# Performance work log

Measured on AMD Instinct MI355X. Metric: run time of the kernel, lower is better.

## Reference

```python
import jax, jax.numpy as jnp
import numpy as np
import math
from jax import lax

K = 5
PAD = K // 2
TAU = 0.1
ALPHA = 2.0
BETA = 1.0
MAXH = math.log(K * K - 1)


def _logp(f):
    # f: [B, d, H, W]; normalize along channels, local kxk affinities (center excluded), log_softmax
    B, d, H, W = f.shape
    nrm = jnp.sqrt(jnp.sum(f * f, axis=1, keepdims=True))
    fn = f / jnp.maximum(nrm, 1e-12)
    fp = jnp.pad(fn, ((0, 0), (0, 0), (PAD, PAD), (PAD, PAD)), mode='reflect')
    center = K * K // 2
    affs = []
    for i in range(K):
        for j in range(K):
            if i * K + j == center:
                continue  # mask removes the center neighbor
            affs.append(jnp.einsum('bdhw,bdhw->bhw', fn, fp[:, :, i:i + H, j:j + W]))
    aff = jnp.stack(affs, axis=-1).reshape(B, H * W, K * K - 1)
    return jax.nn.log_softmax(aff / TAU, axis=-1)


def _sobel_mag(x):
    # x: [B, C, H, W] -> [B, H*W] edge magnitude, per-image min-max normalized
    xm = jnp.mean(x, axis=1, keepdims=True)
    kx = jnp.array([[-1., 0., 1.], [-2., 0., 2.], [-1., 0., 1.]], dtype=x.dtype).reshape(1, 1, 3, 3)
    ky = jnp.array([[-1., -2., -1.], [0., 0., 0.], [1., 2., 1.]], dtype=x.dtype).reshape(1, 1, 3, 3)
    dn = ('NCHW', 'OIHW', 'NCHW')
    gx = lax.conv_general_dilated(xm, kx, (1, 1), 'SAME', dimension_numbers=dn)
    gy = lax.conv_general_dilated(xm, ky, (1, 1), 'SAME', dimension_numbers=dn)
    m = jnp.sqrt(gx * gx + gy * gy)[:, 0]
    mn = jnp.min(m, axis=(1, 2), keepdims=True)
    mx = jnp.max(m, axis=(1, 2), keepdims=True)
    m = (m - mn) / (mx - mn + 1e-6)
    return m.reshape(m.shape[0], -1)


def setup_inputs() -> dict:
    key = jax.random.key(0)
    k1, k2, k3, k4 = jax.random.split(key, 4)
    fs3 = jax.random.normal(k1, (8, 256, 64, 64), dtype=jnp.float32)
    ft = jax.random.normal(k2, (8, 512, 32, 32), dtype=jnp.float32)
    Ws = jax.random.normal(k3, (64, 256), dtype=jnp.float32) / np.sqrt(256.0)
    Wt = jax.random.normal(k4, (64, 512), dtype=jnp.float32) / np.sqrt(512.0)
    return {"fs3": fs3, "ft": ft, "Ws": Ws, "Wt": Wt}


def reference(fs3, ft, Ws, Wt):
    B, _, H, W = fs3.shape
    # bilinear, align_corners=False (half-pixel) == jax.image.resize 'bilinear'
    ft_r = jax.image.resize(ft, (ft.shape[0], ft.shape[1], H, W), method='bilinear')
    s = jnp.einsum('oc,bchw->bohw', Ws, fs3)   # 1x1 conv, no bias
    t = jnp.einsum('oc,bchw->bohw', Wt, ft_r)
    t_logp = _logp(t)
    s_logp = _logp(s)
    # gating weights computed under no_grad in the original
    t_logp_ng = lax.stop_gradient(t_logp)
    t_p = jnp.exp(t_logp_ng)
    ent = -jnp.sum(t_p * t_logp_ng, axis=-1)
    w_conf = jnp.clip(1.0 - ent / (MAXH + 1e-12), 0.0, 1.0)
    w_edge = _sobel_mag(lax.stop_gradient(t))
    w = w_conf ** ALPHA * (1.0 + BETA * w_edge)
    # zero out pad-wide border
    m = jnp.pad(jnp.ones((B, H - 2 * PAD, W - 2 * PAD), dtype=fs3.dtype),
                ((0, 0), (PAD, PAD), (PAD, PAD)))
    w = lax.stop_gradient(w * m.reshape(B, -1))
    kl = jnp.sum(t_p * (t_logp - s_logp), axis=-1)
    return jnp.sum(w * kl) / (jnp.sum(w) + 1e-6)
```

## Files before the change

kernel.cpp:

```cpp
#include <hip/hip_runtime.h>
#include <math.h>


#define WS_T32   0u
#define WS_TN    2097152u
#define WS_SN    4194304u
#define WS_TM    6291456u
#define WS_MAG   6324224u
#define WS_WTT   6356992u
#define WS_WST   6389760u
#define WS_MNMX  6406144u
#define WS_ACC   6406160u
#define WS_SLOGP 0u

static __device__ __forceinline__ int reflect_idx(int i, int n) {
  if (i < 0) i = -i;
  if (i >= n) i = 2 * n - 2 - i;
  return i;
}

__global__ __launch_bounds__(256) void k_transw(const float* __restrict__ Wt,
                                                const float* __restrict__ Ws,
                                                float* __restrict__ WtT,
                                                float* __restrict__ WsT,
                                                unsigned int* __restrict__ mnmx,
                                                double* __restrict__ accg) {
  if (blockIdx.x == 0) {
    int t = threadIdx.x;
    if (t < 8) mnmx[t] = 0x7F800000u;
    else if (t < 16) mnmx[t] = 0u;
    else if (t == 16) { accg[0] = 0.0; accg[1] = 0.0; }
  }
  int idx = blockIdx.x * 256 + threadIdx.x;
  if (idx < 32768) {
    int o = idx >> 9, c = idx & 511;
    WtT[c * 64 + o] = Wt[idx];
  } else {
    int j = idx - 32768;
    int o = j >> 8, c = j & 255;
    WsT[c * 64 + o] = Ws[j];
  }
}

__global__ __launch_bounds__(256) void k_gemm_t(const float* __restrict__ ft,
                                                const float* __restrict__ WtT,
                                                float* __restrict__ t32p) {
  const int tid = threadIdx.x;
  const int wvu = __builtin_amdgcn_readfirstlane(tid >> 6);
  const int ln = tid & 63;
  const int p = blockIdx.x * 64 + ln;
  const int b = p >> 10, pix = p & 1023;
  const int cbase = blockIdx.y * 128;
  float ac[16];
#pragma unroll
  for (int i = 0; i < 16; i++) ac[i] = 0.f;
  const float* ftb = ft + ((size_t)b * 512 + cbase) * 1024 + pix;
  const float* wp = WtT + (size_t)cbase * 64 + wvu * 16;
  for (int c = 0; c < 128; c += 4) {
    float v0 = ftb[(size_t)(c + 0) * 1024];
    float v1 = ftb[(size_t)(c + 1) * 1024];
    float v2 = ftb[(size_t)(c + 2) * 1024];
    float v3 = ftb[(size_t)(c + 3) * 1024];
#pragma unroll
    for (int o = 0; o < 16; o++)
      ac[o] += wp[(c + 0) * 64 + o] * v0 + wp[(c + 1) * 64 + o] * v1
             + wp[(c + 2) * 64 + o] * v2 + wp[(c + 3) * 64 + o] * v3;
  }
  float4* outp = (float4*)(t32p + (size_t)blockIdx.y * 524288
                           + ((size_t)b * 1024 + pix) * 64 + wvu * 16);
#pragma unroll
  for (int j = 0; j < 4; j++)
    outp[j] = make_float4(ac[4 * j], ac[4 * j + 1], ac[4 * j + 2], ac[4 * j + 3]);
}

__global__ __launch_bounds__(128) void k_resize_norm(const float* __restrict__ t32p,
                                                     float* __restrict__ tn,
                                                     float* __restrict__ tm) {
  const int p = blockIdx.x * 128 + threadIdx.x;
  const int b = p >> 12, pix = p & 4095;
  const int y = pix >> 6, x = pix & 63;
  float fy = 0.5f * y - 0.25f, fx = 0.5f * x - 0.25f;
  int y0f = (int)floorf(fy), x0f = (int)floorf(fx);
  float wy = fy - (float)y0f, wx = fx - (float)x0f;
  int y1 = min(y0f + 1, 31), x1 = min(x0f + 1, 31);
  int y0 = max(y0f, 0), x0 = max(x0f, 0);
  const int ip[4] = {y0 * 32 + x0, y0 * 32 + x1, y1 * 32 + x0, y1 * 32 + x1};
  const float wg[4] = {(1.f - wy) * (1.f - wx), (1.f - wy) * wx, wy * (1.f - wx), wy * wx};
  float v[64];
#pragma unroll
  for (int i = 0; i < 64; i++) v[i] = 0.f;
#pragma unroll
  for (int q = 0; q < 4; q++) {
    const float* src = t32p + ((size_t)b * 1024 + ip[q]) * 64;
    float wq = wg[q];
#pragma unroll
    for (int part = 0; part < 4; part++) {
      const float4* s4 = (const float4*)(src + (size_t)part * 524288);
#pragma unroll
      for (int cg = 0; cg < 16; cg++) {
        float4 f = s4[cg];
        v[4 * cg + 0] += wq * f.x; v[4 * cg + 1] += wq * f.y;
        v[4 * cg + 2] += wq * f.z; v[4 * cg + 3] += wq * f.w;
      }
    }
  }
  float sum = 0.f, ssq = 0.f;
#pragma unroll
  for (int i = 0; i < 64; i++) { sum += v[i]; ssq += v[i] * v[i]; }
  float rn = 1.f / fmaxf(sqrtf(ssq), 1e-12f);
  float4* tnp = (float4*)(tn + ((size_t)b * 4096 + pix) * 64);
#pragma unroll
  for (int cg = 0; cg < 16; cg++)
    tnp[cg] = make_float4(v[4 * cg] * rn, v[4 * cg + 1] * rn, v[4 * cg + 2] * rn, v[4 * cg + 3] * rn);
  tm[p] = sum * (1.f / 64.f);
}

__global__ __launch_bounds__(128) void k_sobel(const float* __restrict__ tm,
                                               float* __restrict__ mag,
                                               unsigned int* __restrict__ mnmx) {
  const int p = blockIdx.x * 128 + threadIdx.x;
  const int b = p >> 12, pix = p & 4095;
  const int y = pix >> 6, x = pix & 63;
  const float* img = tm + (size_t)b * 4096;
  float v[3][3];
#pragma unroll
  for (int r = -1; r <= 1; r++)
#pragma unroll
    for (int c = -1; c <= 1; c++) {
      int yy = y + r, xx = x + c;
      v[r + 1][c + 1] = (yy >= 0 && yy < 64 && xx >= 0 && xx < 64) ? img[yy * 64 + xx] : 0.f;
    }
  float gx = (v[0][2] - v[0][0]) + 2.f * (v[1][2] - v[1][0]) + (v[2][2] - v[2][0]);
  float gy = (v[2][0] - v[0][0]) + 2.f * (v[2][1] - v[0][1]) + (v[2][2] - v[0][2]);
  float m = sqrtf(gx * gx + gy * gy);
  mag[p] = m;
  unsigned int mu = __float_as_uint(m);
  unsigned int mnu = mu, mxu = mu;
#pragma unroll
  for (int off = 32; off >= 1; off >>= 1) {
    mnu = min(mnu, __shfl_xor(mnu, off));
    mxu = max(mxu, __shfl_xor(mxu, off));
  }
  if ((threadIdx.x & 63) == 0) {
    atomicMin(&mnmx[b], mnu);
    atomicMax(&mnmx[8 + b], mxu);
  }
}

__global__ __launch_bounds__(256) void k_gemm_s(const float* __restrict__ fs3,
                                                const float* __restrict__ WsT,
                                                float* __restrict__ sn) {
  __shared__ float ssq_l[4][64];
  const int tid = threadIdx.x;
  const int wvu = __builtin_amdgcn_readfirstlane(tid >> 6);
  const int ln = tid & 63;
  const int p = blockIdx.x * 64 + ln;
  const int b = p >> 12, pix = p & 4095;
  float ac[16];
#pragma unroll
  for (int i = 0; i < 16; i++) ac[i] = 0.f;
  const float* fb = fs3 + (size_t)b * 256 * 4096 + pix;
  const float* wp = WsT + wvu * 16;
  for (int c = 0; c < 256; c += 4) {
    float v0 = fb[(size_t)(c + 0) * 4096];
    float v1 = fb[(size_t)(c + 1) * 4096];
    float v2 = fb[(size_t)(c + 2) * 4096];
    float v3 = fb[(size_t)(c + 3) * 4096];
#pragma unroll
    for (int o = 0; o < 16; o++)
      ac[o] += wp[(c + 0) * 64 + o] * v0 + wp[(c + 1) * 64 + o] * v1
             + wp[(c + 2) * 64 + o] * v2 + wp[(c + 3) * 64 + o] * v3;
  }
  float ss = 0.f;
#pragma unroll
  for (int i = 0; i < 16; i++) ss += ac[i] * ac[i];
  ssq_l[wvu][ln] = ss;
  __syncthreads();
  float tot = ssq_l[0][ln] + ssq_l[1][ln] + ssq_l[2][ln] + ssq_l[3][ln];
  float rn = 1.f / fmaxf(sqrtf(tot), 1e-12f);
  float4* ob = (float4*)(sn + ((size_t)b * 4096 + pix) * 64 + wvu * 16);
#pragma unroll
  for (int j = 0; j < 4; j++)
    ob[j] = make_float4(ac[4 * j] * rn, ac[4 * j + 1] * rn, ac[4 * j + 2] * rn, ac[4 * j + 3] * rn);
}

template <int TPASS>
__global__ __launch_bounds__(256) void k_aff(const float* __restrict__ fn,
                                             float* __restrict__ slogp,
                                             const float* __restrict__ mag,
                                             const unsigned int* __restrict__ mnmx,
                                             double* __restrict__ accg) {
  __shared__ __align__(16) float fl[144 * 68];
  const int tid = threadIdx.x;
  const int wvu = __builtin_amdgcn_readfirstlane(tid >> 6);
  const int ln = tid & 63;
  const int b = blockIdx.x >> 6, tl = blockIdx.x & 63;
  const int ty0 = (tl >> 3) * 8, tx0 = (tl & 7) * 8;
  const int ty = ln >> 3, tx = ln & 7;
#pragma unroll
  for (int i = 0; i < 9; i++) {
    int flat = i * 256 + tid;
    int pos = flat >> 4, cg = flat & 15;
    int hy = pos / 12, hx = pos - hy * 12;
    int gy2 = reflect_idx(ty0 + hy - 2, 64);
    int gx2 = reflect_idx(tx0 + hx - 2, 64);
    float4 f = *(const float4*)(fn + ((size_t)b * 4096 + gy2 * 64 + gx2) * 64 + cg * 4);
    int sw = (((pos * 17) >> 3) & 3) << 2;
    *(float4*)(&fl[pos * 68 + ((cg * 4) ^ sw)]) = f;
  }
  __syncthreads();
  const int base = ty * 12 + tx;
  const int cbase = wvu * 16;
  float4 cv[4];
  {
    int cp = base + 26;
    int cs = (((cp * 17) >> 3) & 3) << 2;
    const float* crow = &fl[cp * 68];
#pragma unroll
    for (int j = 0; j < 4; j++) cv[j] = *(const float4*)(crow + ((cbase + 4 * j) ^ cs));
  }
  float aff[24];
  {
    int n = 0;
#pragma unroll
    for (int dy = 0; dy < 5; dy++)
#pragma unroll
      for (int dx = 0; dx < 5; dx++) {
        if (dy == 2 && dx == 2) continue;
        int pp = base + dy * 12 + dx;
        int sw2 = (((pp * 17) >> 3) & 3) << 2;
        const float* rowp = &fl[pp * 68];
        float4 n0 = *(const float4*)(rowp + ((cbase + 0) ^ sw2));
        float4 n1 = *(const float4*)(rowp + ((cbase + 4) ^ sw2));
        float4 n2 = *(const float4*)(rowp + ((cbase + 8) ^ sw2));
        float4 n3 = *(const float4*)(rowp + ((cbase + 12) ^ sw2));
        aff[n] = cv[0].x * n0.x + cv[0].y * n0.y + cv[0].z * n0.z + cv[0].w * n0.w
               + cv[1].x * n1.x + cv[1].y * n1.y + cv[1].z * n1.z + cv[1].w * n1.w
               + cv[2].x * n2.x + cv[2].y * n2.y + cv[2].z * n2.z + cv[2].w * n2.w
               + cv[3].x * n3.x + cv[3].y * n3.y + cv[3].z * n3.z + cv[3].w * n3.w;
        n++;
      }
  }
  __syncthreads();
  float* r = fl;
#pragma unroll
  for (int n = 0; n < 24; n++) r[(wvu * 64 + ln) * 25 + n] = aff[n];
  __syncthreads();
  if (wvu != 0) return;
  float a[24];
#pragma unroll
  for (int n = 0; n < 24; n++)
    a[n] = r[ln * 25 + n] + r[(64 + ln) * 25 + n] + r[(128 + ln) * 25 + n] + r[(192 + ln) * 25 + n];
  float mxa = a[0];
#pragma unroll
  for (int n = 1; n < 24; n++) mxa = fmaxf(mxa, a[n]);
  float e[24]; float sum = 0.f;
#pragma unroll
  for (int n = 0; n < 24; n++) { e[n] = expf((a[n] - mxa) * 10.f); sum += e[n]; }
  float lse = logf(sum);
  const int gy = ty0 + ty, gx = tx0 + tx;
  const int gpix = b * 4096 + gy * 64 + gx;
  if (TPASS == 0) {
#pragma unroll
    for (int n = 0; n < 24; n++)
      slogp[(size_t)n * 32768 + gpix] = (a[n] - mxa) * 10.f - lse;
  } else {
    float rs = 1.f / sum;
    float ent = 0.f, kl = 0.f;
#pragma unroll
    for (int n = 0; n < 24; n++) {
      float tp = e[n] * rs;
      float tlp = (a[n] - mxa) * 10.f - lse;
      ent -= tp * tlp;
      kl += tp * (tlp - slogp[(size_t)n * 32768 + gpix]);
    }
    float wconf = 1.f - ent * (1.0f / 3.17805383034794580f);
    wconf = fminf(fmaxf(wconf, 0.f), 1.f);
    float mnv = __uint_as_float(mnmx[b]);
    float mxv = __uint_as_float(mnmx[8 + b]);
    float wedge = (mag[gpix] - mnv) / (mxv - mnv + 1e-6f);
    float w = wconf * wconf * (1.f + wedge);
    if (gy < 2 || gy >= 62 || gx < 2 || gx >= 62) w = 0.f;
    double wkl = (double)(w * kl), wsum = (double)w;
#pragma unroll
    for (int off = 32; off >= 1; off >>= 1) {
      wkl  += __shfl_down(wkl, off);
      wsum += __shfl_down(wsum, off);
    }
    if (ln == 0) { atomicAdd(&accg[0], wkl); atomicAdd(&accg[1], wsum); }
  }
}

__global__ void k_final(const double* __restrict__ accg, float* __restrict__ out) {
  out[0] = (float)(accg[0] / (accg[1] + 1e-6));
}

extern "C" void kernel_launch(void* const* d_in, const int* in_sizes, int n_in,
                              void* d_out, int out_size, void* d_ws, size_t ws_size,
                              hipStream_t stream) {
  const float* fs3 = (const float*)d_in[0];
  const float* ft  = (const float*)d_in[1];
  const float* Ws  = (const float*)d_in[2];
  const float* Wt  = (const float*)d_in[3];
  float* out = (float*)d_out;
  float* w = (float*)d_ws;
  float* t32   = w + WS_T32;
  float* tn    = w + WS_TN;
  float* sn    = w + WS_SN;
  float* tm    = w + WS_TM;
  float* mag   = w + WS_MAG;
  float* WtT   = w + WS_WTT;
  float* WsT   = w + WS_WST;
  float* slogp = w + WS_SLOGP;
  unsigned int* mnmx = (unsigned int*)(w + WS_MNMX);
  double* acc = (double*)(w + WS_ACC);

  k_transw<<<192, 256, 0, stream>>>(Wt, Ws, WtT, WsT, mnmx, acc);
  k_gemm_t<<<dim3(128, 4), 256, 0, stream>>>(ft, WtT, t32);
  k_resize_norm<<<256, 128, 0, stream>>>(t32, tn, tm);
  k_sobel<<<256, 128, 0, stream>>>(tm, mag, mnmx);
  k_gemm_s<<<512, 256, 0, stream>>>(fs3, WsT, sn);
  k_aff<0><<<512, 256, 0, stream>>>(sn, slogp, nullptr, nullptr, nullptr);
  k_aff<1><<<512, 256, 0, stream>>>(tn, slogp, mag, mnmx, acc);
  k_final<<<1, 1, 0, stream>>>(acc, out);
}
```

Measured before the change: 201.4 us.

## Fuse student/teacher affinity passes, restructure GEMMs and resize, drop final kernel

Merges the two affinity passes into one kernel that stages both student and teacher halos in shared memory. This removes the slogp round trip through global memory and one launch. The final division moves into the last block via an atomic counter, so the separate k_final launch goes away. Both 1x1-conv GEMMs now use 512-thread blocks with 8 outputs per wave and register double-buffered weight and input loads, and the teacher GEMM writes channel-major output. The resize kernel uses 4 threads per pixel with shuffle reductions. The risks are more shared memory per block, which lowers occupancy, and extra atomic ordering logic.

```diff
diff --git a/kernel.cpp b/kernel.cpp
--- a/kernel.cpp
+++ b/kernel.cpp
@@ -10,8 +10,7 @@
 #define WS_WTT   6356992u
 #define WS_WST   6389760u
 #define WS_MNMX  6406144u
-#define WS_ACC   6406160u
-#define WS_SLOGP 0u
+#define WS_ACC   6406168u
 
 static __device__ __forceinline__ int reflect_idx(int i, int n) {
   if (i < 0) i = -i;
@@ -29,7 +28,9 @@
     int t = threadIdx.x;
     if (t < 8) mnmx[t] = 0x7F800000u;
     else if (t < 16) mnmx[t] = 0u;
-    else if (t == 16) { accg[0] = 0.0; accg[1] = 0.0; }
+    else if (t == 16) mnmx[16] = 0u;
+    else if (t == 17) accg[0] = 0.0;
+    else if (t == 18) accg[1] = 0.0;
   }
   int idx = blockIdx.x * 256 + threadIdx.x;
   if (idx < 32768) {
@@ -42,41 +43,66 @@
   }
 }
 
-__global__ __launch_bounds__(256) void k_gemm_t(const float* __restrict__ ft,
-                                                const float* __restrict__ WtT,
-                                                float* __restrict__ t32p) {
+#define LW(WB, CC, A0, A1, B0, B1, C0, C1, D0, D1)                         \
+  { const float4* q0 = (const float4*)((WB) + (CC) * 64);       A0 = q0[0]; A1 = q0[1]; \
+    const float4* q1 = (const float4*)((WB) + ((CC) + 1) * 64); B0 = q1[0]; B1 = q1[1]; \
+    const float4* q2 = (const float4*)((WB) + ((CC) + 2) * 64); C0 = q2[0]; C1 = q2[1]; \
+    const float4* q3 = (const float4*)((WB) + ((CC) + 3) * 64); D0 = q3[0]; D1 = q3[1]; }
+
+#define FMA_GROUP(AC)                                                       \
+  { AC[0] += w00.x * v0 + w10.x * v1 + w20.x * v2 + w30.x * v3;             \
+    AC[1] += w00.y * v0 + w10.y * v1 + w20.y * v2 + w30.y * v3;             \
+    AC[2] += w00.z * v0 + w10.z * v1 + w20.z * v2 + w30.z * v3;             \
+    AC[3] += w00.w * v0 + w10.w * v1 + w20.w * v2 + w30.w * v3;             \
+    AC[4] += w01.x * v0 + w11.x * v1 + w21.x * v2 + w31.x * v3;             \
+    AC[5] += w01.y * v0 + w11.y * v1 + w21.y * v2 + w31.y * v3;             \
+    AC[6] += w01.z * v0 + w11.z * v1 + w21.z * v2 + w31.z * v3;             \
+    AC[7] += w01.w * v0 + w11.w * v1 + w21.w * v2 + w31.w * v3; }
+
+#define ROT8() { w00 = x00; w01 = x01; w10 = x10; w11 = x11;                \
+                 w20 = x20; w21 = x21; w30 = x30; w31 = x31;                \
+                 v0 = u0; v1 = u1; v2 = u2; v3 = u3; }
+
+__global__ __launch_bounds__(512, 4) void k_gemm_t(const float* __restrict__ ft,
+                                                   const float* __restrict__ WtT,
+                                                   float* __restrict__ t32p) {
   const int tid = threadIdx.x;
-  const int wvu = __builtin_amdgcn_readfirstlane(tid >> 6);
-  const int ln = tid & 63;
-  const int p = blockIdx.x * 64 + ln;
-  const int b = p >> 10, pix = p & 1023;
-  const int cbase = blockIdx.y * 128;
-  float ac[16];
-#pragma unroll
-  for (int i = 0; i < 16; i++) ac[i] = 0.f;
-  const float* ftb = ft + ((size_t)b * 512 + cbase) * 1024 + pix;
-  const float* wp = WtT + (size_t)cbase * 64 + wvu * 16;
+  const int w = tid >> 6, ln = tid & 63;
+  const int o0 = __builtin_amdgcn_readfirstlane(w * 8);
+  const int bx = blockIdx.x;
+  const int b = bx >> 4;
+  const int pixl = (bx & 15) * 64 + ln;
+  const int part = blockIdx.y;
+  const float* fb = ft + (size_t)b * 524288 + (size_t)(part * 128) * 1024 + pixl;
+  const float* wb = WtT + (part * 128) * 64 + o0;
+  float ac[8];
+#pragma unroll
+  for (int j = 0; j < 8; j++) ac[j] = 0.f;
+  float4 w00, w01, w10, w11, w20, w21, w30, w31;
+  float v0, v1, v2, v3;
+  LW(wb, 0, w00, w01, w10, w11, w20, w21, w30, w31);
+  { const float* f = fb; v0 = f[0]; v1 = f[1024]; v2 = f[2048]; v3 = f[3072]; }
   for (int c = 0; c < 128; c += 4) {
-    float v0 = ftb[(size_t)(c + 0) * 1024];
-    float v1 = ftb[(size_t)(c + 1) * 1024];
-    float v2 = ftb[(size_t)(c + 2) * 1024];
-    float v3 = ftb[(size_t)(c + 3) * 1024];
-#pragma unroll
-    for (int o = 0; o < 16; o++)
-      ac[o] += wp[(c + 0) * 64 + o] * v0 + wp[(c + 1) * 64 + o] * v1
-             + wp[(c + 2) * 64 + o] * v2 + wp[(c + 3) * 64 + o] * v3;
-  }
-  float4* outp = (float4*)(t32p + (size_t)blockIdx.y * 524288
-                           + ((size_t)b * 1024 + pix) * 64 + wvu * 16);
-#pragma unroll
-  for (int j = 0; j < 4; j++)
-    outp[j] = make_float4(ac[4 * j], ac[4 * j + 1], ac[4 * j + 2], ac[4 * j + 3]);
-}
-
-__global__ __launch_bounds__(128) void k_resize_norm(const float* __restrict__ t32p,
-                                                     float* __restrict__ tn,
-                                                     float* __restrict__ tm) {
-  const int p = blockIdx.x * 128 + threadIdx.x;
+    float4 x00 = {0,0,0,0}, x01 = x00, x10 = x00, x11 = x00, x20 = x00, x21 = x00, x30 = x00, x31 = x00;
+    float u0 = 0.f, u1 = 0.f, u2 = 0.f, u3 = 0.f;
+    if (c + 4 < 128) {
+      LW(wb, c + 4, x00, x01, x10, x11, x20, x21, x30, x31);
+      const float* f = fb + (size_t)(c + 4) * 1024;
+      u0 = f[0]; u1 = f[1024]; u2 = f[2048]; u3 = f[3072];
+    }
+    FMA_GROUP(ac);
+    ROT8();
+  }
+  float* ob = t32p + (((size_t)part * 8 + b) * 64 + o0) * 1024 + pixl;
+#pragma unroll
+  for (int j = 0; j < 8; j++) ob[(size_t)j * 1024] = ac[j];
+}
+
+__global__ __launch_bounds__(256, 4) void k_resize_norm(const float* __restrict__ t32p,
+                                                        float* __restrict__ tn,
+                                                        float* __restrict__ tm) {
+  const int g = blockIdx.x * 256 + threadIdx.x;
+  const int p = g >> 2, q = g & 3;
   const int b = p >> 12, pix = p & 4095;
   const int y = pix >> 6, x = pix & 63;
   float fy = 0.5f * y - 0.25f, fx = 0.5f * x - 0.25f;
@@ -86,33 +112,31 @@
   int y0 = max(y0f, 0), x0 = max(x0f, 0);
   const int ip[4] = {y0 * 32 + x0, y0 * 32 + x1, y1 * 32 + x0, y1 * 32 + x1};
   const float wg[4] = {(1.f - wy) * (1.f - wx), (1.f - wy) * wx, wy * (1.f - wx), wy * wx};
-  float v[64];
-#pragma unroll
-  for (int i = 0; i < 64; i++) v[i] = 0.f;
-#pragma unroll
-  for (int q = 0; q < 4; q++) {
-    const float* src = t32p + ((size_t)b * 1024 + ip[q]) * 64;
-    float wq = wg[q];
+  float v[16];
+#pragma unroll
+  for (int i = 0; i < 16; i++) v[i] = 0.f;
+#pragma unroll
+  for (int cr = 0; cr < 4; cr++) {
+    float wq = wg[cr];
 #pragma unroll
     for (int part = 0; part < 4; part++) {
-      const float4* s4 = (const float4*)(src + (size_t)part * 524288);
-#pragma unroll
-      for (int cg = 0; cg < 16; cg++) {
-        float4 f = s4[cg];
-        v[4 * cg + 0] += wq * f.x; v[4 * cg + 1] += wq * f.y;
-        v[4 * cg + 2] += wq * f.z; v[4 * cg + 3] += wq * f.w;
-      }
+      const float* base = t32p + (((size_t)part * 8 + b) * 64 + q * 16) * 1024 + ip[cr];
+#pragma unroll
+      for (int c = 0; c < 16; c++) v[c] += wq * base[(size_t)c * 1024];
     }
   }
   float sum = 0.f, ssq = 0.f;
 #pragma unroll
-  for (int i = 0; i < 64; i++) { sum += v[i]; ssq += v[i] * v[i]; }
-  float rn = 1.f / fmaxf(sqrtf(ssq), 1e-12f);
-  float4* tnp = (float4*)(tn + ((size_t)b * 4096 + pix) * 64);
-#pragma unroll
-  for (int cg = 0; cg < 16; cg++)
-    tnp[cg] = make_float4(v[4 * cg] * rn, v[4 * cg + 1] * rn, v[4 * cg + 2] * rn, v[4 * cg + 3] * rn);
-  tm[p] = sum * (1.f / 64.f);
+  for (int i = 0; i < 16; i++) { sum += v[i]; ssq += v[i] * v[i]; }
+  float s1 = sum + __shfl_xor(sum, 1);  float sumf = s1 + __shfl_xor(s1, 2);
+  float q1 = ssq + __shfl_xor(ssq, 1);  float ssqf = q1 + __shfl_xor(q1, 2);
+  float rn = 1.f / fmaxf(sqrtf(ssqf), 1e-12f);
+  float* tp = tn + ((size_t)b * 4096 + pix) * 64 + q * 16;
+#pragma unroll
+  for (int j = 0; j < 4; j++)
+    *(float4*)(tp + 4 * j) = make_float4(v[4 * j] * rn, v[4 * j + 1] * rn,
+                                         v[4 * j + 2] * rn, v[4 * j + 3] * rn);
+  if (q == 0) tm[p] = sumf * (1.f / 64.f);
 }
 
 __global__ __launch_bounds__(128) void k_sobel(const float* __restrict__ tm,
@@ -147,50 +171,89 @@
   }
 }
 
-__global__ __launch_bounds__(256) void k_gemm_s(const float* __restrict__ fs3,
-                                                const float* __restrict__ WsT,
-                                                float* __restrict__ sn) {
-  __shared__ float ssq_l[4][64];
+__global__ __launch_bounds__(512, 4) void k_gemm_s(const float* __restrict__ fs3,
+                                                   const float* __restrict__ WsT,
+                                                   float* __restrict__ sn) {
+  __shared__ float ssq_l[8][64];
   const int tid = threadIdx.x;
-  const int wvu = __builtin_amdgcn_readfirstlane(tid >> 6);
-  const int ln = tid & 63;
-  const int p = blockIdx.x * 64 + ln;
-  const int b = p >> 12, pix = p & 4095;
-  float ac[16];
-#pragma unroll
-  for (int i = 0; i < 16; i++) ac[i] = 0.f;
-  const float* fb = fs3 + (size_t)b * 256 * 4096 + pix;
-  const float* wp = WsT + wvu * 16;
+  const int w = tid >> 6, ln = tid & 63;
+  const int o0 = __builtin_amdgcn_readfirstlane(w * 8);
+  const int bx = blockIdx.x;
+  const int b = bx >> 6;
+  const int pixl = (bx & 63) * 64 + ln;
+  const float* fb = fs3 + (size_t)b * 1048576 + pixl;
+  const float* wb = WsT + o0;
+  float ac[8];
+#pragma unroll
+  for (int j = 0; j < 8; j++) ac[j] = 0.f;
+  float4 w00, w01, w10, w11, w20, w21, w30, w31;
+  float v0, v1, v2, v3;
+  LW(wb, 0, w00, w01, w10, w11, w20, w21, w30, w31);
+  { const float* f = fb; v0 = f[0]; v1 = f[4096]; v2 = f[8192]; v3 = f[12288]; }
   for (int c = 0; c < 256; c += 4) {
-    float v0 = fb[(size_t)(c + 0) * 4096];
-    float v1 = fb[(size_t)(c + 1) * 4096];
-    float v2 = fb[(size_t)(c + 2) * 4096];
-    float v3 = fb[(size_t)(c + 3) * 4096];
-#pragma unroll
-    for (int o = 0; o < 16; o++)
-      ac[o] += wp[(c + 0) * 64 + o] * v0 + wp[(c + 1) * 64 + o] * v1
-             + wp[(c + 2) * 64 + o] * v2 + wp[(c + 3) * 64 + o] * v3;
+    float4 x00 = {0,0,0,0}, x01 = x00, x10 = x00, x11 = x00, x20 = x00, x21 = x00, x30 = x00, x31 = x00;
+    float u0 = 0.f, u1 = 0.f, u2 = 0.f, u3 = 0.f;
+    if (c + 4 < 256) {
+      LW(wb, c + 4, x00, x01, x10, x11, x20, x21, x30, x31);
+      const float* f = fb + (size_t)(c + 4) * 4096;
+      u0 = f[0]; u1 = f[4096]; u2 = f[8192]; u3 = f[12288];
+    }
+    FMA_GROUP(ac);
+    ROT8();
   }
   float ss = 0.f;
 #pragma unroll
-  for (int i = 0; i < 16; i++) ss += ac[i] * ac[i];
-  ssq_l[wvu][ln] = ss;
+  for (int j = 0; j < 8; j++) ss += ac[j] * ac[j];
+  ssq_l[w][ln] = ss;
   __syncthreads();
-  float tot = ssq_l[0][ln] + ssq_l[1][ln] + ssq_l[2][ln] + ssq_l[3][ln];
+  float tot = 0.f;
+#pragma unroll
+  for (int j = 0; j < 8; j++) tot += ssq_l[j][ln];
   float rn = 1.f / fmaxf(sqrtf(tot), 1e-12f);
-  float4* ob = (float4*)(sn + ((size_t)b * 4096 + pix) * 64 + wvu * 16);
-#pragma unroll
-  for (int j = 0; j < 4; j++)
-    ob[j] = make_float4(ac[4 * j] * rn, ac[4 * j + 1] * rn, ac[4 * j + 2] * rn, ac[4 * j + 3] * rn);
-}
-
-template <int TPASS>
-__global__ __launch_bounds__(256) void k_aff(const float* __restrict__ fn,
-                                             float* __restrict__ slogp,
-                                             const float* __restrict__ mag,
-                                             const unsigned int* __restrict__ mnmx,
-                                             double* __restrict__ accg) {
-  __shared__ __align__(16) float fl[144 * 68];
+  float* ob = sn + ((size_t)b * 4096 + pixl) * 64 + o0;
+  *(float4*)ob       = make_float4(ac[0] * rn, ac[1] * rn, ac[2] * rn, ac[3] * rn);
+  *(float4*)(ob + 4) = make_float4(ac[4] * rn, ac[5] * rn, ac[6] * rn, ac[7] * rn);
+}
+
+static __device__ __forceinline__ void windows24(const float* flb, int base, int cbase,
+                                                 float* aff) {
+  float4 cv[4];
+  {
+    int cp = base + 26;
+    int cs = (((cp * 17) >> 3) & 3) << 2;
+    const float* crow = flb + cp * 68;
+#pragma unroll
+    for (int j = 0; j < 4; j++) cv[j] = *(const float4*)(crow + ((cbase + 4 * j) ^ cs));
+  }
+  int n = 0;
+#pragma unroll
+  for (int dy = 0; dy < 5; dy++)
+#pragma unroll
+    for (int dx = 0; dx < 5; dx++) {
+      if (dy == 2 && dx == 2) continue;
+      int pp = base + dy * 12 + dx;
+      int sw2 = (((pp * 17) >> 3) & 3) << 2;
+      const float* rowp = flb + pp * 68;
+      float4 q0 = *(const float4*)(rowp + ((cbase + 0) ^ sw2));
+      float4 q1 = *(const float4*)(rowp + ((cbase + 4) ^ sw2));
+      float4 q2 = *(const float4*)(rowp + ((cbase + 8) ^ sw2));
+      float4 q3 = *(const float4*)(rowp + ((cbase + 12) ^ sw2));
+      aff[n] = cv[0].x * q0.x + cv[0].y * q0.y + cv[0].z * q0.z + cv[0].w * q0.w
+             + cv[1].x * q1.x + cv[1].y * q1.y + cv[1].z * q1.z + cv[1].w * q1.w
+             + cv[2].x * q2.x + cv[2].y * q2.y + cv[2].z * q2.z + cv[2].w * q2.w
+             + cv[3].x * q3.x + cv[3].y * q3.y + cv[3].z * q3.z + cv[3].w * q3.w;
+      n++;
+    }
+}
+
+__global__ __launch_bounds__(256, 2) void k_aff(const float* __restrict__ snp,
+                                                const float* __restrict__ tnp,
+                                                const float* __restrict__ mag,
+                                                const unsigned int* __restrict__ mnmx,
+                                                unsigned int* __restrict__ cnt,
+                                                double* __restrict__ accg,
+                                                float* __restrict__ out) {
+  __shared__ __align__(16) float fl[2 * 144 * 68];
   const int tid = threadIdx.x;
   const int wvu = __builtin_amdgcn_readfirstlane(tid >> 6);
   const int ln = tid & 63;
@@ -198,101 +261,90 @@
   const int ty0 = (tl >> 3) * 8, tx0 = (tl & 7) * 8;
   const int ty = ln >> 3, tx = ln & 7;
 #pragma unroll
-  for (int i = 0; i < 9; i++) {
-    int flat = i * 256 + tid;
-    int pos = flat >> 4, cg = flat & 15;
-    int hy = pos / 12, hx = pos - hy * 12;
-    int gy2 = reflect_idx(ty0 + hy - 2, 64);
-    int gx2 = reflect_idx(tx0 + hx - 2, 64);
-    float4 f = *(const float4*)(fn + ((size_t)b * 4096 + gy2 * 64 + gx2) * 64 + cg * 4);
-    int sw = (((pos * 17) >> 3) & 3) << 2;
-    *(float4*)(&fl[pos * 68 + ((cg * 4) ^ sw)]) = f;
+  for (int t2 = 0; t2 < 2; t2++) {
+    const float* src = t2 ? tnp : snp;
+    float* dst = fl + t2 * 9792;
+#pragma unroll
+    for (int i = 0; i < 9; i++) {
+      int flat = i * 256 + tid;
+      int pos = flat >> 4, cg = flat & 15;
+      int hy = pos / 12, hx = pos - hy * 12;
+      int gy2 = reflect_idx(ty0 + hy - 2, 64);
+      int gx2 = reflect_idx(tx0 + hx - 2, 64);
+      float4 f = *(const float4*)(src + ((size_t)b * 4096 + gy2 * 64 + gx2) * 64 + cg * 4);
+      int sw = (((pos * 17) >> 3) & 3) << 2;
+      *(float4*)(&dst[pos * 68 + ((cg * 4) ^ sw)]) = f;
+    }
   }
   __syncthreads();
   const int base = ty * 12 + tx;
   const int cbase = wvu * 16;
-  float4 cv[4];
-  {
-    int cp = base + 26;
-    int cs = (((cp * 17) >> 3) & 3) << 2;
-    const float* crow = &fl[cp * 68];
-#pragma unroll
-    for (int j = 0; j < 4; j++) cv[j] = *(const float4*)(crow + ((cbase + 4 * j) ^ cs));
-  }
-  float aff[24];
-  {
-    int n = 0;
-#pragma unroll
-    for (int dy = 0; dy < 5; dy++)
-#pragma unroll
-      for (int dx = 0; dx < 5; dx++) {
-        if (dy == 2 && dx == 2) continue;
-        int pp = base + dy * 12 + dx;
-        int sw2 = (((pp * 17) >> 3) & 3) << 2;
-        const float* rowp = &fl[pp * 68];
-        float4 n0 = *(const float4*)(rowp + ((cbase + 0) ^ sw2));
-        float4 n1 = *(const float4*)(rowp + ((cbase + 4) ^ sw2));
-        float4 n2 = *(const float4*)(rowp + ((cbase + 8) ^ sw2));
-        float4 n3 = *(const float4*)(rowp + ((cbase + 12) ^ sw2));
-        aff[n] = cv[0].x * n0.x + cv[0].y * n0.y + cv[0].z * n0.z + cv[0].w * n0.w
-               + cv[1].x * n1.x + cv[1].y * n1.y + cv[1].z * n1.z + cv[1].w * n1.w
-               + cv[2].x * n2.x + cv[2].y * n2.y + cv[2].z * n2.z + cv[2].w * n2.w
-               + cv[3].x * n3.x + cv[3].y * n3.y + cv[3].z * n3.z + cv[3].w * n3.w;
-        n++;
-      }
-  }
+  float affs[24], afft[24];
+  windows24(fl, base, cbase, affs);
+  windows24(fl + 9792, base, cbase, afft);
   __syncthreads();
-  float* r = fl;
-#pragma unroll
-  for (int n = 0; n < 24; n++) r[(wvu * 64 + ln) * 25 + n] = aff[n];
+  float* rs = fl;
+  float* rt = fl + 6400;
+#pragma unroll
+  for (int n = 0; n < 24; n++) {
+    rs[(wvu * 64 + ln) * 25 + n] = affs[n];
+    rt[(wvu * 64 + ln) * 25 + n] = afft[n];
+  }
   __syncthreads();
   if (wvu != 0) return;
-  float a[24];
-#pragma unroll
-  for (int n = 0; n < 24; n++)
-    a[n] = r[ln * 25 + n] + r[(64 + ln) * 25 + n] + r[(128 + ln) * 25 + n] + r[(192 + ln) * 25 + n];
-  float mxa = a[0];
-#pragma unroll
-  for (int n = 1; n < 24; n++) mxa = fmaxf(mxa, a[n]);
-  float e[24]; float sum = 0.f;
-#pragma unroll
-  for (int n = 0; n < 24; n++) { e[n] = expf((a[n] - mxa) * 10.f); sum += e[n]; }
-  float lse = logf(sum);
+  float as_[24], at_[24];
+#pragma unroll
+  for (int n = 0; n < 24; n++) {
+    as_[n] = rs[ln * 25 + n] + rs[(64 + ln) * 25 + n] + rs[(128 + ln) * 25 + n] + rs[(192 + ln) * 25 + n];
+    at_[n] = rt[ln * 25 + n] + rt[(64 + ln) * 25 + n] + rt[(128 + ln) * 25 + n] + rt[(192 + ln) * 25 + n];
+  }
+  float mxt = at_[0], mxs = as_[0];
+#pragma unroll
+  for (int n = 1; n < 24; n++) { mxt = fmaxf(mxt, at_[n]); mxs = fmaxf(mxs, as_[n]); }
+  float et[24];
+  float st = 0.f, ssum = 0.f;
+#pragma unroll
+  for (int n = 0; n < 24; n++) {
+    et[n] = expf((at_[n] - mxt) * 10.f); st += et[n];
+    ssum += expf((as_[n] - mxs) * 10.f);
+  }
+  float lset = logf(st), lses = logf(ssum);
+  float rst = 1.f / st;
+  float ent = 0.f, kl = 0.f;
+#pragma unroll
+  for (int n = 0; n < 24; n++) {
+    float tp = et[n] * rst;
+    float tlp = (at_[n] - mxt) * 10.f - lset;
+    float slp = (as_[n] - mxs) * 10.f - lses;
+    ent -= tp * tlp;
+    kl += tp * (tlp - slp);
+  }
+  float wconf = 1.f - ent * (1.0f / 3.17805383034794580f);
+  wconf = fminf(fmaxf(wconf, 0.f), 1.f);
   const int gy = ty0 + ty, gx = tx0 + tx;
   const int gpix = b * 4096 + gy * 64 + gx;
-  if (TPASS == 0) {
-#pragma unroll
-    for (int n = 0; n < 24; n++)
-      slogp[(size_t)n * 32768 + gpix] = (a[n] - mxa) * 10.f - lse;
-  } else {
-    float rs = 1.f / sum;
-    float ent = 0.f, kl = 0.f;
-#pragma unroll
-    for (int n = 0; n < 24; n++) {
-      float tp = e[n] * rs;
-      float tlp = (a[n] - mxa) * 10.f - lse;
-      ent -= tp * tlp;
-      kl += tp * (tlp - slogp[(size_t)n * 32768 + gpix]);
-    }
-    float wconf = 1.f - ent * (1.0f / 3.17805383034794580f);
-    wconf = fminf(fmaxf(wconf, 0.f), 1.f);
-    float mnv = __uint_as_float(mnmx[b]);
-    float mxv = __uint_as_float(mnmx[8 + b]);
-    float wedge = (mag[gpix] - mnv) / (mxv - mnv + 1e-6f);
-    float w = wconf * wconf * (1.f + wedge);
-    if (gy < 2 || gy >= 62 || gx < 2 || gx >= 62) w = 0.f;
-    double wkl = (double)(w * kl), wsum = (double)w;
-#pragma unroll
-    for (int off = 32; off >= 1; off >>= 1) {
-      wkl  += __shfl_down(wkl, off);
-      wsum += __shfl_down(wsum, off);
-    }
-    if (ln == 0) { atomicAdd(&accg[0], wkl); atomicAdd(&accg[1], wsum); }
-  }
-}
-
-__global__ void k_final(const double* __restrict__ accg, float* __restrict__ out) {
-  out[0] = (float)(accg[0] / (accg[1] + 1e-6));
+  float mnv = __uint_as_float(mnmx[b]);
+  float mxv = __uint_as_float(mnmx[8 + b]);
+  float wedge = (mag[gpix] - mnv) / (mxv - mnv + 1e-6f);
+  float wgt = wconf * wconf * (1.f + wedge);
+  if (gy < 2 || gy >= 62 || gx < 2 || gx >= 62) wgt = 0.f;
+  double wkl = (double)(wgt * kl), wsum = (double)wgt;
+#pragma unroll
+  for (int off = 32; off >= 1; off >>= 1) {
+    wkl  += __shfl_down(wkl, off);
+    wsum += __shfl_down(wsum, off);
+  }
+  if (ln == 0) {
+    atomicAdd(&accg[0], wkl);
+    atomicAdd(&accg[1], wsum);
+    __threadfence();
+    unsigned int old = atomicAdd(cnt, 1u);
+    if (old == 511u) {
+      double a0 = atomicAdd(&accg[0], 0.0);
+      double a1 = atomicAdd(&accg[1], 0.0);
+      out[0] = (float)(a0 / (a1 + 1e-6));
+    }
+  }
 }
 
 extern "C" void kernel_launch(void* const* d_in, const int* in_sizes, int n_in,
@@ -304,23 +356,20 @@
   const float* Wt  = (const float*)d_in[3];
   float* out = (float*)d_out;
   float* w = (float*)d_ws;
-  float* t32   = w + WS_T32;
-  float* tn    = w + WS_TN;
-  float* sn    = w + WS_SN;
-  float* tm    = w + WS_TM;
-  float* mag   = w + WS_MAG;
-  float* WtT   = w + WS_WTT;
-  float* WsT   = w + WS_WST;
-  float* slogp = w + WS_SLOGP;
+  float* t32 = w + WS_T32;
+  float* tn  = w + WS_TN;
+  float* sn  = w + WS_SN;
+  float* tm  = w + WS_TM;
+  float* mag = w + WS_MAG;
+  float* WtT = w + WS_WTT;
+  float* WsT = w + WS_WST;
   unsigned int* mnmx = (unsigned int*)(w + WS_MNMX);
   double* acc = (double*)(w + WS_ACC);
 
   k_transw<<<192, 256, 0, stream>>>(Wt, Ws, WtT, WsT, mnmx, acc);
-  k_gemm_t<<<dim3(128, 4), 256, 0, stream>>>(ft, WtT, t32);
-  k_resize_norm<<<256, 128, 0, stream>>>(t32, tn, tm);
+  k_gemm_t<<<dim3(128, 4), 512, 0, stream>>>(ft, WtT, t32);
+  k_resize_norm<<<512, 256, 0, stream>>>(t32, tn, tm);
   k_sobel<<<256, 128, 0, stream>>>(tm, mag, mnmx);
-  k_gemm_s<<<512, 256, 0, stream>>>(fs3, WsT, sn);
-  k_aff<0><<<512, 256, 0, stream>>>(sn, slogp, nullptr, nullptr, nullptr);
-  k_aff<1><<<512, 256, 0, stream>>>(tn, slogp, mag, mnmx, acc);
-  k_final<<<1, 1, 0, stream>>>(acc, out);
-}
+  k_gemm_s<<<512, 512, 0, stream>>>(fs3, WsT, sn);
+  k_aff<<<512, 256, 0, stream>>>(sn, tn, mag, mnmx, &mnmx[16], acc, out);
+}
```

Result: no change. 200.4 us (-0.5%).
